# Performance work log

Hardware: AMD Instinct MI355X
Metric: run time of the kernel (lower is better)

The kernel has to match this reference:

```python
import jax, jax.numpy as jnp
import numpy as np

D_EMB = 1024
B, T = 8, 2048

def setup_inputs() -> dict:
    key = jax.random.key(0)
    ks = jax.random.split(key, 7)
    s = 0.02
    return {
        "x": jax.random.normal(ks[0], (B, T, D_EMB), dtype=jnp.float32),
        "W_attn": jax.random.normal(ks[1], (3 * D_EMB, D_EMB), dtype=jnp.float32) * s,
        "b_attn": jax.random.normal(ks[2], (3 * D_EMB,), dtype=jnp.float32) * s,
        "W_proj": jax.random.normal(ks[3], (D_EMB, D_EMB), dtype=jnp.float32) * s,
        "b_proj": jax.random.normal(ks[4], (D_EMB,), dtype=jnp.float32) * s,
        "W_fc": jax.random.normal(ks[5], (1, D_EMB), dtype=jnp.float32) * s,
        "b_fc": jax.random.normal(ks[6], (1,), dtype=jnp.float32) * s,
    }

def reference(x, W_attn, b_attn, W_proj, b_proj, W_fc, b_fc):
    # qkv projection: torch Linear => x @ W.T + b
    qkv = jnp.einsum('btc,dc->btd', x, W_attn) + b_attn          # [B,T,3C]
    q, k, v = jnp.split(qkv, 3, axis=2)                          # each [B,T,C]
    scale = q.shape[-1] ** (-0.5)
    attn_scores = jnp.einsum('btc,bsc->bts', q, k) * scale       # [B,T,T]
    attn_weights = jax.nn.softmax(attn_scores, axis=-1)          # traditional softmax
    y = jnp.einsum('bts,bsc->btc', attn_weights, v)              # [B,T,C]
    y = jnp.einsum('btc,dc->btd', y, W_proj) + b_proj            # [B,T,C]
    out = jnp.einsum('btc,oc->bto', y, W_fc) + b_fc              # [B,T,1]
    return out
```

## Files before the change

### kernel.cpp

```cpp
#include <hip/hip_runtime.h>
#include <stdint.h>

#define D_EMB 1024
#define NBATCH 8
#define SEQ 2048
#define MTOT (NBATCH*SEQ)

typedef __attribute__((ext_vector_type(8))) short short8;
typedef __attribute__((ext_vector_type(4))) float f32x4;

__device__ __forceinline__ ushort bf16r(float x) {
  union { float f; uint32_t u; } c; c.f = x;
  return (ushort)((c.u + 0x7fffu + ((c.u >> 16) & 1u)) >> 16);
}

__device__ __forceinline__ void cp16(const ushort* g, ushort* l) {
  __builtin_amdgcn_global_load_lds(
      (const __attribute__((address_space(1))) void*)g,
      (__attribute__((address_space(3))) void*)l, 16, 0, 0);
}

__global__ void cvt_kernel(const float4* __restrict__ in, ushort* __restrict__ out, long n4) {
  long i = blockIdx.x * (long)blockDim.x + threadIdx.x;
  long stride = (long)gridDim.x * blockDim.x;
  for (; i < n4; i += stride) {
    float4 v = in[i];
    ushort4 o = make_ushort4(bf16r(v.x), bf16r(v.y), bf16r(v.z), bf16r(v.w));
    *(ushort4*)(out + i * 4) = o;
  }
}

__global__ __launch_bounds__(256) void cvt_x_vw(
    const float4* __restrict__ x4, const float4* __restrict__ wv4,
    const float* __restrict__ sc, ushort* __restrict__ xb, float* __restrict__ vw) {
  int wave = threadIdx.x >> 6, lane = threadIdx.x & 63;
  long row = (long)blockIdx.x * 4 + wave;
  const float4* xr = x4 + row * 256;
  ushort* xo = xb + row * D_EMB;
  float s = 0.f;
  #pragma unroll
  for (int i = 0; i < 4; i++) {
    int idx = lane + i * 64;
    float4 v = xr[idx];
    float4 w = wv4[idx];
    *(ushort4*)(xo + idx * 4) = make_ushort4(bf16r(v.x), bf16r(v.y), bf16r(v.z), bf16r(v.w));
    s += v.x * w.x + v.y * w.y + v.z * w.z + v.w * w.w;
  }
  #pragma unroll
  for (int off = 32; off; off >>= 1) s += __shfl_xor(s, off);
  if (lane == 0) vw[row] = s + sc[1];
}

__global__ void init_kernel(const float* __restrict__ bp, const float* __restrict__ Wfc,
                            const float* __restrict__ bfc,
                            float* __restrict__ w_eff, float* __restrict__ wv_eff,
                            float* __restrict__ numden, float* __restrict__ sc) {
  int tid = threadIdx.x;
  int b = blockIdx.x;
  if (b == 0) { w_eff[tid] = 0.f; return; }
  if (b == 1) { wv_eff[tid] = 0.f; return; }
  if (b >= 3) { numden[(long)(b - 3) * 1024 + tid] = 0.f; return; }
  float v = bp[tid] * Wfc[tid];
  int lane = tid & 63, w = tid >> 6;
  #pragma unroll
  for (int off = 32; off; off >>= 1) v += __shfl_xor(v, off);
  __shared__ float red[16];
  if (lane == 0) red[w] = v;
  __syncthreads();
  if (tid == 0) {
    float s = 0.f;
    #pragma unroll
    for (int i = 0; i < 16; i++) s += red[i];
    sc[0] = s + bfc[0];
  }
}

__global__ void prep1(const float* __restrict__ Wp, const float* __restrict__ Wfc,
                      float* __restrict__ w_eff) {
  int c = blockIdx.x * 256 + threadIdx.x;
  int d0 = blockIdx.y * 16;
  float s = 0.f;
  #pragma unroll
  for (int d = d0; d < d0 + 16; d++) s += Wfc[d] * Wp[(long)d * D_EMB + c];
  atomicAdd(&w_eff[c], s);
}

__global__ void prep2(const float* __restrict__ Wattn, const float* __restrict__ battn,
                      const float* __restrict__ w_eff, float* __restrict__ wv_eff,
                      float* __restrict__ sc) {
  int tid = threadIdx.x;
  if (blockIdx.y == 64) {
    if (blockIdx.x != 0) return;
    float v = 0.f;
    #pragma unroll
    for (int i = 0; i < 4; i++) { int c = tid + i * 256; v += battn[2048 + c] * w_eff[c]; }
    int lane = tid & 63, w = tid >> 6;
    #pragma unroll
    for (int off = 32; off; off >>= 1) v += __shfl_xor(v, off);
    __shared__ float red[4];
    if (lane == 0) red[w] = v;
    __syncthreads();
    if (tid == 0) sc[1] = red[0] + red[1] + red[2] + red[3];
    return;
  }
  int d = blockIdx.x * 256 + tid;
  int c0 = blockIdx.y * 16;
  float s = 0.f;
  #pragma unroll
  for (int c = c0; c < c0 + 16; c++) s += w_eff[c] * Wattn[(long)(2048 + c) * D_EMB + d];
  atomicAdd(&wv_eff[d], s);
}

template<bool FUSED>
__global__ __launch_bounds__(256, 4) void gemm_nt(
    const ushort* __restrict__ A, long lda, long sAz,
    const ushort* __restrict__ B, long ldb, long sBz,
    ushort* __restrict__ C, long ldc,
    const float* __restrict__ bias, float scale, int K,
    const float* __restrict__ vw, float* __restrict__ num, float* __restrict__ den) {
  __shared__ __align__(16) ushort lds_a[128 * 64];
  __shared__ __align__(16) ushort lds_b[128 * 64];
  int z = blockIdx.z;
  const ushort* Az = A + (long)z * sAz;
  const ushort* Bz = B + (long)z * sBz;
  long m0 = (long)blockIdx.y * 128, n0 = (long)blockIdx.x * 128;
  int t = threadIdx.x;
  int wave = t >> 6, lane = t & 63;
  int r = lane & 15, q = lane >> 4;
  int wm = (wave & 1) * 64, wn = (wave >> 1) * 64;

  f32x4 acc[4][4] = {};

  int row0 = t >> 3;
  int kc = (t & 7) ^ (row0 & 7);
  const ushort* Ap = Az + (m0 + row0) * lda + kc * 8;
  const ushort* Bp = Bz + (n0 + row0) * ldb + kc * 8;
  long a32 = 32 * lda, b32 = 32 * ldb;

  int swz = r & 7;

  #pragma unroll 1
  for (int k0 = 0; k0 < K; k0 += 64) {
    if (k0) __syncthreads();
    cp16(Ap + k0,            lds_a + t * 8);
    cp16(Ap + k0 + a32,      lds_a + (t + 256) * 8);
    cp16(Ap + k0 + 2 * a32,  lds_a + (t + 512) * 8);
    cp16(Ap + k0 + 3 * a32,  lds_a + (t + 768) * 8);
    cp16(Bp + k0,            lds_b + t * 8);
    cp16(Bp + k0 + b32,      lds_b + (t + 256) * 8);
    cp16(Bp + k0 + 2 * b32,  lds_b + (t + 512) * 8);
    cp16(Bp + k0 + 3 * b32,  lds_b + (t + 768) * 8);
    __syncthreads();
    #pragma unroll
    for (int kk = 0; kk < 2; kk++) {
      int cidx = (kk * 4 + q) ^ swz;
      short8 af[4], bf[4];
      #pragma unroll
      for (int i = 0; i < 4; i++)
        af[i] = *(const short8*)(lds_a + ((wm + i * 16 + r) * 8 + cidx) * 8);
      #pragma unroll
      for (int j = 0; j < 4; j++)
        bf[j] = *(const short8*)(lds_b + ((wn + j * 16 + r) * 8 + cidx) * 8);
      #pragma unroll
      for (int i = 0; i < 4; i++)
        #pragma unroll
        for (int j = 0; j < 4; j++)
          acc[i][j] = __builtin_amdgcn_mfma_f32_16x16x32_bf16(af[i], bf[j], acc[i][j], 0, 0, 0);
    }
  }

  if (!FUSED) {
    #pragma unroll
    for (int i = 0; i < 4; i++) {
      #pragma unroll
      for (int j = 0; j < 4; j++) {
        long col = n0 + wn + j * 16 + r;
        float bj = bias[col];
        #pragma unroll
        for (int rr = 0; rr < 4; rr++) {
          long row = m0 + wm + i * 16 + q * 4 + rr;
          C[row * ldc + col] = bf16r(acc[i][j][rr] * scale + bj);
        }
      }
    }
  } else {
    const float* vwz = vw + (long)z * SEQ + n0;
    float* numz = num + (long)z * SEQ + m0;
    float* denz = den + (long)z * SEQ + m0;
    float vwj[4];
    #pragma unroll
    for (int j = 0; j < 4; j++) vwj[j] = vwz[wn + j * 16 + r];
    #pragma unroll
    for (int i = 0; i < 4; i++) {
      #pragma unroll
      for (int rr = 0; rr < 4; rr++) {
        float sn = 0.f, sd = 0.f;
        #pragma unroll
        for (int j = 0; j < 4; j++) {
          float e = __expf(acc[i][j][rr] * scale);
          sd += e;
          sn += e * vwj[j];
        }
        #pragma unroll
        for (int off = 1; off < 16; off <<= 1) {
          sn += __shfl_xor(sn, off);
          sd += __shfl_xor(sd, off);
        }
        if (r == 0) {
          int row = wm + i * 16 + q * 4 + rr;
          atomicAdd(&numz[row], sn);
          atomicAdd(&denz[row], sd);
        }
      }
    }
  }
}

__global__ __launch_bounds__(256) void finalize(
    const float* __restrict__ num, const float* __restrict__ den,
    const float* __restrict__ sc, float* __restrict__ out) {
  long i = blockIdx.x * 256L + threadIdx.x;
  out[i] = num[i] / den[i] + sc[0];
}

extern "C" void kernel_launch(void* const* d_in, const int* in_sizes, int n_in,
                              void* d_out, int out_size, void* d_ws, size_t ws_size,
                              hipStream_t stream) {
  const float* x     = (const float*)d_in[0];
  const float* Wattn = (const float*)d_in[1];
  const float* battn = (const float*)d_in[2];
  const float* Wproj = (const float*)d_in[3];
  const float* bproj = (const float*)d_in[4];
  const float* Wfc   = (const float*)d_in[5];
  const float* bfc   = (const float*)d_in[6];
  float* out = (float*)d_out;

  const size_t OFF_XB    = 0;
  const size_t OFF_WQKB  = 33554432;
  const size_t OFF_QK    = 37748736;
  const size_t OFF_NUM   = 104857600;
  const size_t OFF_DEN   = 104923136;
  const size_t OFF_VW    = 104988672;
  const size_t OFF_WEFF  = 105054208;
  const size_t OFF_WVEFF = 105058304;
  const size_t OFF_SC    = 105062400;
  const size_t NEED      = 105062408;
  if (ws_size < NEED) return;

  char* ws = (char*)d_ws;
  ushort* xb    = (ushort*)(ws + OFF_XB);
  ushort* wqkb  = (ushort*)(ws + OFF_WQKB);
  ushort* qk    = (ushort*)(ws + OFF_QK);
  float* num    = (float*)(ws + OFF_NUM);
  float* den    = (float*)(ws + OFF_DEN);
  float* vw     = (float*)(ws + OFF_VW);
  float* w_eff  = (float*)(ws + OFF_WEFF);
  float* wv_eff = (float*)(ws + OFF_WVEFF);
  float* sc     = (float*)(ws + OFF_SC);

  init_kernel<<<dim3(35), dim3(1024), 0, stream>>>(bproj, Wfc, bfc, w_eff, wv_eff, num, sc);
  prep1<<<dim3(4, 64), dim3(256), 0, stream>>>(Wproj, Wfc, w_eff);
  prep2<<<dim3(4, 65), dim3(256), 0, stream>>>(Wattn, battn, w_eff, wv_eff, sc);

  cvt_kernel<<<dim3(2048), dim3(256), 0, stream>>>((const float4*)Wattn, wqkb, (long)2048 * D_EMB / 4);
  cvt_x_vw<<<dim3(4096), dim3(256), 0, stream>>>((const float4*)x, (const float4*)wv_eff, sc, xb, vw);

  gemm_nt<false><<<dim3(16, 128, 1), dim3(256), 0, stream>>>(
      xb, (long)D_EMB, 0L, wqkb, (long)D_EMB, 0L,
      qk, 2048L, battn, 1.0f, D_EMB, nullptr, nullptr, nullptr);

  gemm_nt<true><<<dim3(16, 16, NBATCH), dim3(256), 0, stream>>>(
      qk, 2048L, (long)SEQ * 2048, qk + 1024, 2048L, (long)SEQ * 2048,
      nullptr, 0L, nullptr, 0.03125f, D_EMB, vw, num, den);

  finalize<<<dim3(64), dim3(256), 0, stream>>>(num, den, sc, out);
}
```

Measured before the change: 271.3 us.

## Switch GEMMs to 32x32x16 MFMA, remap blocks per XCD, fuse conversion kernels

Replaces the 16x16x32 bf16 MFMA tiling with 32x32x16 MFMA (2x2 accumulators of 16 floats per wave), changes the LDS XOR swizzle to suit the new access pattern, and remaps block indices so blocks of the same batch or row band land on the same XCD for better L2 reuse. It also merges the weight and x bf16 conversion kernels into one launch. The fused epilogue now reduces across 32 lanes instead of 16. These aim to cut LDS read traffic per MFMA, improve cache locality, and remove a launch, at the risk of bank conflicts if the new swizzle is wrong and slightly longer shuffle reductions.

```diff
diff --git a/kernel.cpp b/kernel.cpp
--- a/kernel.cpp
+++ b/kernel.cpp
@@ -7,7 +7,7 @@
 #define MTOT (NBATCH*SEQ)
 
 typedef __attribute__((ext_vector_type(8))) short short8;
-typedef __attribute__((ext_vector_type(4))) float f32x4;
+typedef __attribute__((ext_vector_type(16))) float f32x16;
 
 __device__ __forceinline__ ushort bf16r(float x) {
   union { float f; uint32_t u; } c; c.f = x;
@@ -20,35 +20,37 @@
       (__attribute__((address_space(3))) void*)l, 16, 0, 0);
 }
 
-__global__ void cvt_kernel(const float4* __restrict__ in, ushort* __restrict__ out, long n4) {
-  long i = blockIdx.x * (long)blockDim.x + threadIdx.x;
-  long stride = (long)gridDim.x * blockDim.x;
-  for (; i < n4; i += stride) {
-    float4 v = in[i];
-    ushort4 o = make_ushort4(bf16r(v.x), bf16r(v.y), bf16r(v.z), bf16r(v.w));
-    *(ushort4*)(out + i * 4) = o;
-  }
-}
-
-__global__ __launch_bounds__(256) void cvt_x_vw(
-    const float4* __restrict__ x4, const float4* __restrict__ wv4,
-    const float* __restrict__ sc, ushort* __restrict__ xb, float* __restrict__ vw) {
-  int wave = threadIdx.x >> 6, lane = threadIdx.x & 63;
-  long row = (long)blockIdx.x * 4 + wave;
-  const float4* xr = x4 + row * 256;
-  ushort* xo = xb + row * D_EMB;
-  float s = 0.f;
-  #pragma unroll
-  for (int i = 0; i < 4; i++) {
-    int idx = lane + i * 64;
-    float4 v = xr[idx];
-    float4 w = wv4[idx];
-    *(ushort4*)(xo + idx * 4) = make_ushort4(bf16r(v.x), bf16r(v.y), bf16r(v.z), bf16r(v.w));
-    s += v.x * w.x + v.y * w.y + v.z * w.z + v.w * w.w;
-  }
-  #pragma unroll
-  for (int off = 32; off; off >>= 1) s += __shfl_xor(s, off);
-  if (lane == 0) vw[row] = s + sc[1];
+__global__ __launch_bounds__(256) void cvt_all(
+    const float4* __restrict__ x4, const float4* __restrict__ W4,
+    const float4* __restrict__ wv4, const float* __restrict__ sc,
+    ushort* __restrict__ xb, ushort* __restrict__ wqkb, float* __restrict__ vw) {
+  int tid = threadIdx.x;
+  if (blockIdx.x < 4096) {
+    int wave = tid >> 6, lane = tid & 63;
+    long row = (long)blockIdx.x * 4 + wave;
+    const float4* xr = x4 + row * 256;
+    ushort* xo = xb + row * D_EMB;
+    float s = 0.f;
+    #pragma unroll
+    for (int i = 0; i < 4; i++) {
+      int idx = lane + i * 64;
+      float4 v = xr[idx];
+      float4 w = wv4[idx];
+      *(ushort4*)(xo + idx * 4) = make_ushort4(bf16r(v.x), bf16r(v.y), bf16r(v.z), bf16r(v.w));
+      s += v.x * w.x + v.y * w.y + v.z * w.z + v.w * w.w;
+    }
+    #pragma unroll
+    for (int off = 32; off; off >>= 1) s += __shfl_xor(s, off);
+    if (lane == 0) vw[row] = s + sc[1];
+  } else {
+    long base = (long)(blockIdx.x - 4096) * 1024 + tid;
+    #pragma unroll
+    for (int i = 0; i < 4; i++) {
+      long idx = base + i * 256;
+      float4 v = W4[idx];
+      *(ushort4*)(wqkb + idx * 4) = make_ushort4(bf16r(v.x), bf16r(v.y), bf16r(v.z), bf16r(v.w));
+    }
+  }
 }
 
 __global__ void init_kernel(const float* __restrict__ bp, const float* __restrict__ Wfc,
@@ -120,66 +122,74 @@
     const float* __restrict__ vw, float* __restrict__ num, float* __restrict__ den) {
   __shared__ __align__(16) ushort lds_a[128 * 64];
   __shared__ __align__(16) ushort lds_b[128 * 64];
-  int z = blockIdx.z;
+
+  long f = blockIdx.x + 16L * blockIdx.y + (FUSED ? 256L * blockIdx.z : 0L);
+  int xcd = (int)(f & 7);
+  long g = f >> 3;
+  int bx = (int)(g & 15);
+  int by, z;
+  if (FUSED) { z = xcd; by = (int)(g >> 4); }
+  else       { z = 0;   by = xcd * 16 + (int)(g >> 4); }
+
   const ushort* Az = A + (long)z * sAz;
   const ushort* Bz = B + (long)z * sBz;
-  long m0 = (long)blockIdx.y * 128, n0 = (long)blockIdx.x * 128;
+  long m0 = (long)by * 128, n0 = (long)bx * 128;
   int t = threadIdx.x;
   int wave = t >> 6, lane = t & 63;
-  int r = lane & 15, q = lane >> 4;
+  int c = lane & 31, h = lane >> 5;
   int wm = (wave & 1) * 64, wn = (wave >> 1) * 64;
 
-  f32x4 acc[4][4] = {};
+  f32x16 acc[2][2] = {};
 
   int row0 = t >> 3;
-  int kc = (t & 7) ^ (row0 & 7);
+  int kc = (t & 7) ^ (((row0 >> 2) ^ row0) & 7);
   const ushort* Ap = Az + (m0 + row0) * lda + kc * 8;
   const ushort* Bp = Bz + (n0 + row0) * ldb + kc * 8;
   long a32 = 32 * lda, b32 = 32 * ldb;
 
-  int swz = r & 7;
+  int swz = ((c >> 2) ^ c) & 7;
 
   #pragma unroll 1
   for (int k0 = 0; k0 < K; k0 += 64) {
     if (k0) __syncthreads();
-    cp16(Ap + k0,            lds_a + t * 8);
-    cp16(Ap + k0 + a32,      lds_a + (t + 256) * 8);
-    cp16(Ap + k0 + 2 * a32,  lds_a + (t + 512) * 8);
-    cp16(Ap + k0 + 3 * a32,  lds_a + (t + 768) * 8);
-    cp16(Bp + k0,            lds_b + t * 8);
-    cp16(Bp + k0 + b32,      lds_b + (t + 256) * 8);
-    cp16(Bp + k0 + 2 * b32,  lds_b + (t + 512) * 8);
-    cp16(Bp + k0 + 3 * b32,  lds_b + (t + 768) * 8);
+    cp16(Ap + k0,           lds_a + t * 8);
+    cp16(Ap + k0 + a32,     lds_a + (t + 256) * 8);
+    cp16(Ap + k0 + 2 * a32, lds_a + (t + 512) * 8);
+    cp16(Ap + k0 + 3 * a32, lds_a + (t + 768) * 8);
+    cp16(Bp + k0,           lds_b + t * 8);
+    cp16(Bp + k0 + b32,     lds_b + (t + 256) * 8);
+    cp16(Bp + k0 + 2 * b32, lds_b + (t + 512) * 8);
+    cp16(Bp + k0 + 3 * b32, lds_b + (t + 768) * 8);
     __syncthreads();
     #pragma unroll
-    for (int kk = 0; kk < 2; kk++) {
-      int cidx = (kk * 4 + q) ^ swz;
-      short8 af[4], bf[4];
-      #pragma unroll
-      for (int i = 0; i < 4; i++)
-        af[i] = *(const short8*)(lds_a + ((wm + i * 16 + r) * 8 + cidx) * 8);
-      #pragma unroll
-      for (int j = 0; j < 4; j++)
-        bf[j] = *(const short8*)(lds_b + ((wn + j * 16 + r) * 8 + cidx) * 8);
-      #pragma unroll
-      for (int i = 0; i < 4; i++)
-        #pragma unroll
-        for (int j = 0; j < 4; j++)
-          acc[i][j] = __builtin_amdgcn_mfma_f32_16x16x32_bf16(af[i], bf[j], acc[i][j], 0, 0, 0);
+    for (int ks = 0; ks < 4; ks++) {
+      int cidx = (2 * ks + h) ^ swz;
+      short8 af[2], bf[2];
+      #pragma unroll
+      for (int i = 0; i < 2; i++)
+        af[i] = *(const short8*)(lds_a + ((wm + i * 32 + c) * 8 + cidx) * 8);
+      #pragma unroll
+      for (int j = 0; j < 2; j++)
+        bf[j] = *(const short8*)(lds_b + ((wn + j * 32 + c) * 8 + cidx) * 8);
+      #pragma unroll
+      for (int i = 0; i < 2; i++)
+        #pragma unroll
+        for (int j = 0; j < 2; j++)
+          acc[i][j] = __builtin_amdgcn_mfma_f32_32x32x16_bf16(af[i], bf[j], acc[i][j], 0, 0, 0);
     }
   }
 
   if (!FUSED) {
     #pragma unroll
-    for (int i = 0; i < 4; i++) {
-      #pragma unroll
-      for (int j = 0; j < 4; j++) {
-        long col = n0 + wn + j * 16 + r;
+    for (int i = 0; i < 2; i++) {
+      #pragma unroll
+      for (int j = 0; j < 2; j++) {
+        long col = n0 + wn + j * 32 + c;
         float bj = bias[col];
         #pragma unroll
-        for (int rr = 0; rr < 4; rr++) {
-          long row = m0 + wm + i * 16 + q * 4 + rr;
-          C[row * ldc + col] = bf16r(acc[i][j][rr] * scale + bj);
+        for (int reg = 0; reg < 16; reg++) {
+          long row = m0 + wm + i * 32 + (reg & 3) + 8 * (reg >> 2) + 4 * h;
+          C[row * ldc + col] = bf16r(acc[i][j][reg] * scale + bj);
         }
       }
     }
@@ -187,27 +197,27 @@
     const float* vwz = vw + (long)z * SEQ + n0;
     float* numz = num + (long)z * SEQ + m0;
     float* denz = den + (long)z * SEQ + m0;
-    float vwj[4];
-    #pragma unroll
-    for (int j = 0; j < 4; j++) vwj[j] = vwz[wn + j * 16 + r];
-    #pragma unroll
-    for (int i = 0; i < 4; i++) {
-      #pragma unroll
-      for (int rr = 0; rr < 4; rr++) {
+    float vwj[2];
+    #pragma unroll
+    for (int j = 0; j < 2; j++) vwj[j] = vwz[wn + j * 32 + c];
+    #pragma unroll
+    for (int i = 0; i < 2; i++) {
+      #pragma unroll
+      for (int reg = 0; reg < 16; reg++) {
         float sn = 0.f, sd = 0.f;
         #pragma unroll
-        for (int j = 0; j < 4; j++) {
-          float e = __expf(acc[i][j][rr] * scale);
+        for (int j = 0; j < 2; j++) {
+          float e = __expf(acc[i][j][reg] * scale);
           sd += e;
           sn += e * vwj[j];
         }
         #pragma unroll
-        for (int off = 1; off < 16; off <<= 1) {
+        for (int off = 1; off < 32; off <<= 1) {
           sn += __shfl_xor(sn, off);
           sd += __shfl_xor(sd, off);
         }
-        if (r == 0) {
-          int row = wm + i * 16 + q * 4 + rr;
+        if (c == 0) {
+          int row = wm + i * 32 + (reg & 3) + 8 * (reg >> 2) + 4 * h;
           atomicAdd(&numz[row], sn);
           atomicAdd(&denz[row], sd);
         }
@@ -262,8 +272,8 @@
   prep1<<<dim3(4, 64), dim3(256), 0, stream>>>(Wproj, Wfc, w_eff);
   prep2<<<dim3(4, 65), dim3(256), 0, stream>>>(Wattn, battn, w_eff, wv_eff, sc);
 
-  cvt_kernel<<<dim3(2048), dim3(256), 0, stream>>>((const float4*)Wattn, wqkb, (long)2048 * D_EMB / 4);
-  cvt_x_vw<<<dim3(4096), dim3(256), 0, stream>>>((const float4*)x, (const float4*)wv_eff, sc, xb, vw);
+  cvt_all<<<dim3(4096 + 512), dim3(256), 0, stream>>>(
+      (const float4*)x, (const float4*)Wattn, (const float4*)wv_eff, sc, xb, wqkb, vw);
 
   gemm_nt<false><<<dim3(16, 128, 1), dim3(256), 0, stream>>>(
       xb, (long)D_EMB, 0L, wqkb, (long)D_EMB, 0L,
```

After: 340.3 us. 25.4% more time.
